# Kernel optimization log

Measured on AMD Instinct MI355X. Metric: run time of the kernel, lower is better.

Reference implementation:

```python
import jax, jax.numpy as jnp
import numpy as np
import math

DEGREE = 4   # MacLaurin expansion degree
FEAT = 8     # input feature dim F
BATCH = 65536


def _build_terms_facs():
    """Enumerate all exponent multi-indices with total degree <= DEGREE,
    mirroring the TF meshgrid construction, plus 1/k! factors per term."""
    d1 = DEGREE + 1
    grids = np.meshgrid(*([np.arange(d1)] * FEAT), indexing='ij')
    terms = np.stack(grids, axis=-1).reshape(-1, FEAT)           # [(d+1)^F, F]
    terms = terms[terms.sum(axis=-1) <= DEGREE]                  # [T, F], T = C(F+d, d)
    fact = np.array([math.factorial(k) for k in range(d1)], dtype=np.float32)
    facs = (1.0 / fact)[terms.sum(axis=-1)]                      # [T] = 1/|alpha|!
    return jnp.asarray(terms, dtype=jnp.float32), jnp.asarray(facs, dtype=jnp.float32)


def setup_inputs() -> dict:
    key = jax.random.key(0)
    k1, k2 = jax.random.split(key)
    terms, facs = _build_terms_facs()
    T = terms.shape[0]  # 495
    x = jax.random.uniform(k1, (BATCH, FEAT), dtype=jnp.float32)  # positive inputs (pow-safe)
    coefs = jax.random.normal(k2, (1, T), dtype=jnp.float32) * 0.05
    return {"x": x, "terms": terms, "coefs": coefs, "facs": facs}


def reference(x, terms, coefs, facs):
    # monomials: prod_f x[b,f]^terms[t,f]  -> [B, T]
    mono = jnp.prod(x[:, None, :] ** terms[None, :, :], axis=-1)
    # weighted sum over terms: sum_t facs[t] * coefs[0,t] * mono[b,t] -> [B]
    return jnp.sum(facs * coefs * mono, axis=-1)
```

## Files before the change

kernel.cpp:

```cpp
#include <hip/hip_runtime.h>

#define NF 8
#define DEG 4
#define NTERMS 495

template<int F, int REM> struct Node;
template<int F, int REM, int E> struct Branch;

template<int F, int REM>
struct Node {
    static __device__ __forceinline__ void run(const float* xs, const float* w,
                                               int& t, float p,
                                               float& a0, float& a1) {
        Branch<F, REM, 0>::run(xs, w, t, p, a0, a1);
    }
};

template<int REM>
struct Node<NF, REM> {
    static __device__ __forceinline__ void run(const float* , const float* w,
                                               int& t, float p,
                                               float& a0, float& a1) {
        a0 = fmaf(w[t], p, a0);
        ++t;
    }
};

template<int F, int REM, int E>
struct Branch {
    static __device__ __forceinline__ void run(const float* xs, const float* w,
                                               int& t, float pf,
                                               float& a0, float& a1) {
        Node<F + 1, REM - E>::run(xs, w, t, pf, a0, a1);
        if constexpr (E < REM) {
            Branch<F, REM, E + 1>::run(xs, w, t, pf * xs[F], a1, a0);
        }
    }
};

__global__ __launch_bounds__(256)
void maclaurin_fused(const float* __restrict__ x,
                     const float* __restrict__ coefs,
                     const float* __restrict__ facs,
                     float* __restrict__ out, int n) {
    __shared__ __align__(16) float wl[NTERMS];

    const int tid = threadIdx.x;
    const int b   = blockIdx.x * blockDim.x + tid;

    float xs[NF];
    if (b < n) {
        const float4* xp = (const float4*)(x + (size_t)b * NF);
        float4 v0 = xp[0];
        float4 v1 = xp[1];
        xs[0] = v0.x; xs[1] = v0.y; xs[2] = v0.z; xs[3] = v0.w;
        xs[4] = v1.x; xs[5] = v1.y; xs[6] = v1.z; xs[7] = v1.w;
    }

    if (tid < NTERMS)       wl[tid]       = coefs[tid]       * facs[tid];
    if (tid + 256 < NTERMS) wl[tid + 256] = coefs[tid + 256] * facs[tid + 256];
    __syncthreads();

    if (b >= n) return;

    float a0 = 0.0f, a1 = 0.0f;
    int t = 0;
    Node<0, DEG>::run(xs, wl, t, 1.0f, a0, a1);

    out[b] = a0 + a1;
}

extern "C" void kernel_launch(void* const* d_in, const int* in_sizes, int n_in,
                              void* d_out, int out_size, void* d_ws, size_t ws_size,
                              hipStream_t stream) {
    const float* x     = (const float*)d_in[0];
    const float* coefs = (const float*)d_in[2];
    const float* facs  = (const float*)d_in[3];
    float* out = (float*)d_out;

    int n = in_sizes[0] / NF;

    maclaurin_fused<<<(n + 255) / 256, 256, 0, stream>>>(x, coefs, facs, out, n);
}
```

Before: 11.11 us.

## Split term tree across four waves per element and reduce partials in LDS

Each block now processes 64 elements. The four wavefronts each evaluate a compile-time slice of the 495-term monomial tree for the same elements. Partial sums go to shared memory and are combined by the first wave. This shortens each thread's serial dependency chain and launches four times more blocks for better CU occupancy. In exchange, x is loaded redundantly, the coefficient table is built in more blocks, and an extra barrier plus LDS reduction is added.

```diff
diff --git a/kernel.cpp b/kernel.cpp
--- a/kernel.cpp
+++ b/kernel.cpp
@@ -3,40 +3,57 @@
 #define NF 8
 #define DEG 4
 #define NTERMS 495
+#define NPART 4
+#define EPB 64
 
-template<int F, int REM> struct Node;
-template<int F, int REM, int E> struct Branch;
+constexpr long long nCkll(int n, int k) {
+    long long r = 1;
+    for (int i = 1; i <= k; ++i) r = r * (n - k + i) / i;
+    return r;
+}
+constexpr int subcnt(int F, int REM) { return (int)nCkll(NF - F + REM, REM); }
 
-template<int F, int REM>
+template<int F, int REM, int T0, int LO, int HI> struct Node;
+template<int F, int REM, int E, int T0, int LO, int HI> struct Branch;
+
+template<int F, int REM, int T0, int LO, int HI>
 struct Node {
     static __device__ __forceinline__ void run(const float* xs, const float* w,
-                                               int& t, float p,
-                                               float& a0, float& a1) {
-        Branch<F, REM, 0>::run(xs, w, t, p, a0, a1);
+                                               float p, float& a0, float& a1) {
+        if constexpr (T0 + subcnt(F, REM) <= LO || T0 >= HI) {
+            (void)xs; (void)w; (void)p; (void)a0; (void)a1;
+        } else {
+            Branch<F, REM, 0, T0, LO, HI>::run(xs, w, p, a0, a1);
+        }
     }
 };
 
-template<int REM>
-struct Node<NF, REM> {
-    static __device__ __forceinline__ void run(const float* , const float* w,
-                                               int& t, float p,
-                                               float& a0, float& a1) {
-        a0 = fmaf(w[t], p, a0);
-        ++t;
+template<int REM, int T0, int LO, int HI>
+struct Node<NF, REM, T0, LO, HI> {
+    static __device__ __forceinline__ void run(const float*, const float* w,
+                                               float p, float& a0, float& a1) {
+        (void)a1;
+        if constexpr (T0 >= LO && T0 < HI) {
+            a0 = fmaf(w[T0], p, a0);
+        } else {
+            (void)w; (void)p; (void)a0;
+        }
     }
 };
 
-template<int F, int REM, int E>
+template<int F, int REM, int E, int T0, int LO, int HI>
 struct Branch {
+    static constexpr int childCnt = subcnt(F + 1, REM - E);
     static __device__ __forceinline__ void run(const float* xs, const float* w,
-                                               int& t, float pf,
-                                               float& a0, float& a1) {
-        Node<F + 1, REM - E>::run(xs, w, t, pf, a0, a1);
+                                               float pf, float& a0, float& a1) {
+        Node<F + 1, REM - E, T0, LO, HI>::run(xs, w, pf, a0, a1);
         if constexpr (E < REM) {
-            Branch<F, REM, E + 1>::run(xs, w, t, pf * xs[F], a1, a0);
+            Branch<F, REM, E + 1, T0 + childCnt, LO, HI>::run(xs, w, pf * xs[F], a1, a0);
         }
     }
 };
+
+#define PB(p) ((p) * NTERMS / NPART)
 
 __global__ __launch_bounds__(256)
 void maclaurin_fused(const float* __restrict__ x,
@@ -44,30 +61,46 @@
                      const float* __restrict__ facs,
                      float* __restrict__ out, int n) {
     __shared__ __align__(16) float wl[NTERMS];
+    __shared__ float partial[NPART][EPB];
 
-    const int tid = threadIdx.x;
-    const int b   = blockIdx.x * blockDim.x + tid;
+    const int tid  = threadIdx.x;
+    const int lane = tid & 63;
+    const int part = tid >> 6;
+    const int elem = blockIdx.x * EPB + lane;
 
     float xs[NF];
-    if (b < n) {
-        const float4* xp = (const float4*)(x + (size_t)b * NF);
+    if (elem < n) {
+        const float4* xp = (const float4*)(x + (size_t)elem * NF);
         float4 v0 = xp[0];
         float4 v1 = xp[1];
         xs[0] = v0.x; xs[1] = v0.y; xs[2] = v0.z; xs[3] = v0.w;
         xs[4] = v1.x; xs[5] = v1.y; xs[6] = v1.z; xs[7] = v1.w;
+    } else {
+        #pragma unroll
+        for (int f = 0; f < NF; ++f) xs[f] = 0.0f;
     }
 
     if (tid < NTERMS)       wl[tid]       = coefs[tid]       * facs[tid];
     if (tid + 256 < NTERMS) wl[tid + 256] = coefs[tid + 256] * facs[tid + 256];
     __syncthreads();
 
-    if (b >= n) return;
+    float a0 = 0.0f, a1 = 0.0f;
+    switch (part) {
+        case 0: Node<0, DEG, 0, PB(0), PB(1)>::run(xs, wl, 1.0f, a0, a1); break;
+        case 1: Node<0, DEG, 0, PB(1), PB(2)>::run(xs, wl, 1.0f, a0, a1); break;
+        case 2: Node<0, DEG, 0, PB(2), PB(3)>::run(xs, wl, 1.0f, a0, a1); break;
+        default:Node<0, DEG, 0, PB(3), PB(4)>::run(xs, wl, 1.0f, a0, a1); break;
+    }
+    partial[part][lane] = a0 + a1;
+    __syncthreads();
 
-    float a0 = 0.0f, a1 = 0.0f;
-    int t = 0;
-    Node<0, DEG>::run(xs, wl, t, 1.0f, a0, a1);
-
-    out[b] = a0 + a1;
+    if (tid < EPB) {
+        int e = blockIdx.x * EPB + tid;
+        if (e < n) {
+            out[e] = (partial[0][tid] + partial[1][tid])
+                   + (partial[2][tid] + partial[3][tid]);
+        }
+    }
 }
 
 extern "C" void kernel_launch(void* const* d_in, const int* in_sizes, int n_in,
@@ -79,6 +112,7 @@
     float* out = (float*)d_out;
 
     int n = in_sizes[0] / NF;
+    int grid = (n + EPB - 1) / EPB;
 
-    maclaurin_fused<<<(n + 255) / 256, 256, 0, stream>>>(x, coefs, facs, out, n);
+    maclaurin_fused<<<grid, 256, 0, stream>>>(x, coefs, facs, out, n);
 }
```

Measured after the change: 13.56 us. +22.1%, slower.
